# Performance work log

Hardware: AMD Instinct MI355X
Metric: run time of the kernel (lower is better)

## Reference

```python
import jax, jax.numpy as jnp
import numpy as np

M_DIM = 256.0  # scaling denominator from __init__ (sqrt(256) = 16)

def setup_inputs() -> dict:
    key = jax.random.key(0)
    kq, kk, kv = jax.random.split(key, 3)
    B, H, S, D = 2, 8, 4096, 64
    q = jax.random.normal(kq, (B, H, S, D), dtype=jnp.float32)
    k = jax.random.normal(kk, (B, H, S, D), dtype=jnp.float32)
    v = jax.random.normal(kv, (B, H, S, D), dtype=jnp.float32)
    return {"q": q, "k": k, "v": v}

def reference(q, k, v):
    # scores: [B, H, S, S] = q @ k^T / sqrt(m_dim)
    scores = jnp.einsum('bhqd,bhkd->bhqk', q, k) / jnp.sqrt(jnp.float32(M_DIM))
    attn = jax.nn.softmax(scores, axis=-1)
    # outputs: [B, H, S, D]
    return jnp.einsum('bhqk,bhkd->bhqd', attn, v)
```

## Files before the change

kernel.cpp:

```cpp
#include <hip/hip_runtime.h>
#include <hip/hip_bf16.h>
#include <stdint.h>

#define SEQ 4096
#define DH  64
#define KT  32
#define PS  40
#define NIT ((SEQ / 4) / KT)
#define QSCALE 0.090168440f

typedef __attribute__((ext_vector_type(8))) short short8;
typedef __attribute__((ext_vector_type(4))) float floatx4;

__device__ __forceinline__ ushort f2bf_rne(float f) {
    unsigned u = __float_as_uint(f);
    unsigned r = u + 0x7FFFu + ((u >> 16) & 1u);
    return (ushort)(r >> 16);
}

__global__ __launch_bounds__(256)
void prep_kv(const float* __restrict__ K, const float* __restrict__ V,
             ushort* __restrict__ Kf, ushort* __restrict__ Vf) {
    const int bh = blockIdx.y, kb0 = blockIdx.x * 128, t = threadIdx.x;
    const size_t inB = ((size_t)bh * SEQ + kb0) * DH;
    {
        const float* srcB = K + inB;
        ushort* dstB = Kf + (size_t)bh * SEQ * DH + (size_t)(kb0 >> 4) * 1024;
        #pragma unroll
        for (int p = 0; p < 4; ++p) {
            int c   = p * 256 + t;
            int g   = c >> 7, rem = c & 127;
            int tt  = rem >> 6, lam = rem & 63;
            int key = g * 16 + (lam & 15);
            int d0  = tt * 32 + (lam >> 4) * 8;
            const float* s = srcB + (size_t)key * DH + d0;
            float4 a = *(const float4*)s;
            float4 b = *(const float4*)(s + 4);
            short8 o;
            o[0] = (short)f2bf_rne(a.x); o[1] = (short)f2bf_rne(a.y);
            o[2] = (short)f2bf_rne(a.z); o[3] = (short)f2bf_rne(a.w);
            o[4] = (short)f2bf_rne(b.x); o[5] = (short)f2bf_rne(b.y);
            o[6] = (short)f2bf_rne(b.z); o[7] = (short)f2bf_rne(b.w);
            *(short8*)(dstB + g * 1024 + tt * 512 + lam * 8) = o;
        }
    }
    {
        const int d0 = (t & 15) * 4, sl = (t >> 4) * 8;
        const float* src = V + inB + (size_t)sl * DH + d0;
        ushort* dstB = Vf + (size_t)bh * SEQ * DH + (size_t)(kb0 >> 5) * 2048;
        ushort b[8][4];
        #pragma unroll
        for (int r = 0; r < 8; ++r) {
            float4 f = *(const float4*)(src + r * DH);
            b[r][0] = f2bf_rne(f.x); b[r][1] = f2bf_rne(f.y);
            b[r][2] = f2bf_rne(f.z); b[r][3] = f2bf_rne(f.w);
        }
        const int Tl = sl >> 5, kq = (sl & 31) >> 3;
        #pragma unroll
        for (int i = 0; i < 4; ++i) {
            int d = d0 + i;
            short8 w;
            #pragma unroll
            for (int r = 0; r < 8; ++r) w[r] = (short)b[r][i];
            *(short8*)(dstB + Tl * 2048 + (d >> 4) * 512 + kq * 128 + (d & 15) * 8) = w;
        }
    }
}

__global__ __launch_bounds__(256, 4)
void attn_fwd_v14(const float* __restrict__ Q, const ushort* __restrict__ Kf,
                  const ushort* __restrict__ Vf, float* __restrict__ O)
{
    __shared__ __align__(16) char smem[35328];

    const int g    = blockIdx.x;
    const int bh   = (g & 7) * 2 + ((g >> 3) & 1);
    const int qt0  = (g >> 4) * 64;

    const int tid   = threadIdx.x;
    const int wave  = tid >> 6;
    const int lane  = tid & 63;
    const int n16   = lane & 15;
    const int quad  = lane >> 4;

    const float* Qb  = Q + ((size_t)bh * SEQ) * DH;
    const char*  KfB = (const char*)(Kf + (size_t)bh * SEQ * DH);
    const char*  VfB = (const char*)(Vf + (size_t)bh * SEQ * DH);
    float*       Ob  = O + ((size_t)bh * SEQ) * DH;

    ushort* sPw = (ushort*)smem + wave * (64 * PS);
    ushort* sQ  = (ushort*)(smem + 20480);

    #pragma unroll
    for (int p = 0; p < 2; ++p) {
        int c   = p * 256 + tid;
        int qt  = c >> 7, rem = c & 127;
        int tt  = rem >> 6, lam = rem & 63;
        int row = qt0 + qt * 16 + (lam & 15);
        int d0  = tt * 32 + (lam >> 4) * 8;
        const float* s = Qb + (size_t)row * DH + d0;
        float4 a = *(const float4*)s;
        float4 b = *(const float4*)(s + 4);
        short8 o;
        o[0] = (short)f2bf_rne(a.x * QSCALE); o[1] = (short)f2bf_rne(a.y * QSCALE);
        o[2] = (short)f2bf_rne(a.z * QSCALE); o[3] = (short)f2bf_rne(a.w * QSCALE);
        o[4] = (short)f2bf_rne(b.x * QSCALE); o[5] = (short)f2bf_rne(b.y * QSCALE);
        o[6] = (short)f2bf_rne(b.z * QSCALE); o[7] = (short)f2bf_rne(b.w * QSCALE);
        *(short8*)(sQ + qt * 1024 + tt * 512 + lam * 8) = o;
    }

    floatx4 oacc[4][4];
    float   lpart[4];
    #pragma unroll
    for (int qt = 0; qt < 4; ++qt) {
        lpart[qt] = 0.f;
        #pragma unroll
        for (int nt = 0; nt < 4; ++nt) oacc[qt][nt] = (floatx4){0.f, 0.f, 0.f, 0.f};
    }

    const int wqoff = __builtin_amdgcn_readfirstlane(wave * 131072);
    const char* kpB = KfB + wqoff;
    const char* vpB = VfB + wqoff;
    const int lo = lane * 16;

    short8 kf[4];
    #pragma unroll
    for (int c = 0; c < 4; ++c) kf[c] = *(const short8*)(kpB + lo + c * 1024);

    __syncthreads();

    const ushort* sQl = sQ + lane * 8;

    int off = 0;
    #pragma unroll 1
    for (int it = 0; it < NIT; ++it) {
        asm volatile("" ::: "memory");

        const int offn = (it + 1 < NIT) ? off + 4096 : 0;

        #pragma unroll
        for (int qt = 0; qt < 4; ++qt) {
            short8 q0 = *(const short8*)(sQl + qt * 1024);
            short8 q1 = *(const short8*)(sQl + qt * 1024 + 512);
            floatx4 s0 = (floatx4){0.f, 0.f, 0.f, 0.f};
            floatx4 s1 = (floatx4){0.f, 0.f, 0.f, 0.f};
            __builtin_amdgcn_s_setprio(1);
            s0 = __builtin_amdgcn_mfma_f32_16x16x32_bf16(kf[0], q0, s0, 0, 0, 0);
            s0 = __builtin_amdgcn_mfma_f32_16x16x32_bf16(kf[1], q1, s0, 0, 0, 0);
            s1 = __builtin_amdgcn_mfma_f32_16x16x32_bf16(kf[2], q0, s1, 0, 0, 0);
            s1 = __builtin_amdgcn_mfma_f32_16x16x32_bf16(kf[3], q1, s1, 0, 0, 0);
            __builtin_amdgcn_s_setprio(0);
            {
                float e0 = __builtin_amdgcn_exp2f(s0[0]);
                float e1 = __builtin_amdgcn_exp2f(s0[1]);
                float e2 = __builtin_amdgcn_exp2f(s0[2]);
                float e3 = __builtin_amdgcn_exp2f(s0[3]);
                lpart[qt] += (e0 + e1) + (e2 + e3);
                uint2 w;
                w.x = __builtin_amdgcn_perm(__float_as_uint(e1), __float_as_uint(e0), 0x07060302);
                w.y = __builtin_amdgcn_perm(__float_as_uint(e3), __float_as_uint(e2), 0x07060302);
                *(uint2*)&sPw[(qt * 16 + n16) * PS + quad * 4] = w;
            }
            {
                float e0 = __builtin_amdgcn_exp2f(s1[0]);
                float e1 = __builtin_amdgcn_exp2f(s1[1]);
                float e2 = __builtin_amdgcn_exp2f(s1[2]);
                float e3 = __builtin_amdgcn_exp2f(s1[3]);
                lpart[qt] += (e0 + e1) + (e2 + e3);
                uint2 w;
                w.x = __builtin_amdgcn_perm(__float_as_uint(e1), __float_as_uint(e0), 0x07060302);
                w.y = __builtin_amdgcn_perm(__float_as_uint(e3), __float_as_uint(e2), 0x07060302);
                *(uint2*)&sPw[(qt * 16 + n16) * PS + 16 + quad * 4] = w;
            }
        }

        asm volatile("" ::: "memory");

        short8 vf[4];
        #pragma unroll
        for (int c = 0; c < 4; ++c) vf[c] = *(const short8*)(vpB + lo + off + c * 1024);

        #pragma unroll
        for (int c = 0; c < 4; ++c) kf[c] = *(const short8*)(kpB + lo + offn + c * 1024);

        #pragma unroll
        for (int qt = 0; qt < 4; ++qt) {
            short8 pfq = *(const short8*)&sPw[(qt * 16 + n16) * PS + quad * 8];
            __builtin_amdgcn_s_setprio(1);
            #pragma unroll
            for (int nt = 0; nt < 4; ++nt)
                oacc[qt][nt] = __builtin_amdgcn_mfma_f32_16x16x32_bf16(vf[nt], pfq, oacc[qt][nt], 0, 0, 0);
            __builtin_amdgcn_s_setprio(0);
        }

        off = offn;
    }

    float lq[4];
    #pragma unroll
    for (int qt = 0; qt < 4; ++qt) {
        float s = lpart[qt];
        s += __shfl_xor(s, 16, 64);
        s += __shfl_xor(s, 32, 64);
        lq[qt] = s;
    }

    __syncthreads();
    if (wave & 1) {
        char* rb = smem + (wave >> 1) * 17664;
        float* eO = (float*)rb;
        float* eL = (float*)(rb + 17408);
        #pragma unroll
        for (int qt = 0; qt < 4; ++qt) {
            const int row = qt * 16 + n16;
            #pragma unroll
            for (int nt = 0; nt < 4; ++nt)
                *(float4*)&eO[row * 68 + nt * 16 + quad * 4] = (float4){
                    oacc[qt][nt][0], oacc[qt][nt][1], oacc[qt][nt][2], oacc[qt][nt][3]};
            if (quad == 0) eL[row] = lq[qt];
        }
    }
    __syncthreads();
    if (!(wave & 1)) {
        const char* rb = smem + (wave >> 1) * 17664;
        const float* eO = (const float*)rb;
        const float* eL = (const float*)(rb + 17408);
        #pragma unroll
        for (int qt = 0; qt < 4; ++qt) {
            const int row = qt * 16 + n16;
            lq[qt] += eL[row];
            #pragma unroll
            for (int nt = 0; nt < 4; ++nt) {
                float4 part = *(const float4*)&eO[row * 68 + nt * 16 + quad * 4];
                oacc[qt][nt][0] += part.x; oacc[qt][nt][1] += part.y;
                oacc[qt][nt][2] += part.z; oacc[qt][nt][3] += part.w;
            }
        }
    }
    __syncthreads();
    if (wave == 2) {
        char* rb = smem;
        float* eO = (float*)rb;
        float* eL = (float*)(rb + 17408);
        #pragma unroll
        for (int qt = 0; qt < 4; ++qt) {
            const int row = qt * 16 + n16;
            #pragma unroll
            for (int nt = 0; nt < 4; ++nt)
                *(float4*)&eO[row * 68 + nt * 16 + quad * 4] = (float4){
                    oacc[qt][nt][0], oacc[qt][nt][1], oacc[qt][nt][2], oacc[qt][nt][3]};
            if (quad == 0) eL[row] = lq[qt];
        }
    }
    __syncthreads();
    if (wave == 0) {
        const float* eO = (const float*)smem;
        const float* eL = (const float*)(smem + 17408);
        #pragma unroll
        for (int qt = 0; qt < 4; ++qt) {
            const int row = qt * 16 + n16;
            const float inv = 1.0f / (lq[qt] + eL[row]);
            const int q = qt0 + row;
            #pragma unroll
            for (int nt = 0; nt < 4; ++nt) {
                float4 part = *(const float4*)&eO[row * 68 + nt * 16 + quad * 4];
                float4 o;
                o.x = (oacc[qt][nt][0] + part.x) * inv;
                o.y = (oacc[qt][nt][1] + part.y) * inv;
                o.z = (oacc[qt][nt][2] + part.z) * inv;
                o.w = (oacc[qt][nt][3] + part.w) * inv;
                *(float4*)&Ob[(size_t)q * DH + nt * 16 + quad * 4] = o;
            }
        }
    }
}

__global__ __launch_bounds__(256, 4)
void attn_fwd_v1(const float* __restrict__ Q, const float* __restrict__ K,
                 const float* __restrict__ V, float* __restrict__ O)
{
    __shared__ __align__(16) ushort sKf[64 * 72];
    __shared__ __align__(16) ushort sVf[64 * 72];
    __shared__ __align__(16) ushort sPf[4 * 16 * 72];
    const int bh = blockIdx.y, qt0 = blockIdx.x * 64, tid = threadIdx.x;
    const int wave = tid >> 6, lane = tid & 63, n16 = lane & 15, quad = lane >> 4;
    const size_t base = (size_t)bh * SEQ * DH;
    const float *Qb = Q + base, *Kb = K + base, *Vb = V + base;
    float* Ob = O + base;
    short8 qfrag[2];
    {
        const float* qrow = Qb + (size_t)(qt0 + wave * 16 + n16) * DH;
        #pragma unroll
        for (int t = 0; t < 2; ++t) {
            const float* p = qrow + t * 32 + quad * 8;
            short8 a;
            #pragma unroll
            for (int j = 0; j < 8; ++j) a[j] = (short)f2bf_rne(p[j] * 0.0625f);
            qfrag[t] = a;
        }
    }
    floatx4 oacc[4];
    #pragma unroll
    for (int nt = 0; nt < 4; ++nt) oacc[nt] = (floatx4){0.f,0.f,0.f,0.f};
    float m_i[4] = {-INFINITY,-INFINITY,-INFINITY,-INFINITY};
    float l_i[4] = {0.f,0.f,0.f,0.f};
    const int skr = tid >> 2, sc0 = (tid & 3) * 16;
    for (int kt0 = 0; kt0 < SEQ; kt0 += 64) {
        __syncthreads();
        const float* ksrc = Kb + (size_t)(kt0 + skr) * DH + sc0;
        const float* vsrc = Vb + (size_t)(kt0 + skr) * DH + sc0;
        ushort* kdst = &sKf[skr * 72 + sc0];
        #pragma unroll
        for (int i = 0; i < 16; i += 4) {
            float4 kf = *(const float4*)(ksrc + i);
            kdst[i+0]=f2bf_rne(kf.x); kdst[i+1]=f2bf_rne(kf.y);
            kdst[i+2]=f2bf_rne(kf.z); kdst[i+3]=f2bf_rne(kf.w);
            float4 vf = *(const float4*)(vsrc + i);
            sVf[(sc0+i+0)*72+skr]=f2bf_rne(vf.x); sVf[(sc0+i+1)*72+skr]=f2bf_rne(vf.y);
            sVf[(sc0+i+2)*72+skr]=f2bf_rne(vf.z); sVf[(sc0+i+3)*72+skr]=f2bf_rne(vf.w);
        }
        __syncthreads();
        floatx4 sacc[4];
        #pragma unroll
        for (int nt = 0; nt < 4; ++nt) {
            sacc[nt] = (floatx4){0.f,0.f,0.f,0.f};
            #pragma unroll
            for (int t = 0; t < 2; ++t) {
                short8 b = *(const short8*)&sKf[(nt*16+n16)*72 + t*32 + quad*8];
                sacc[nt] = __builtin_amdgcn_mfma_f32_16x16x32_bf16(qfrag[t], b, sacc[nt], 0,0,0);
            }
        }
        ushort* pw = &sPf[wave * 16 * 72];
        #pragma unroll
        for (int r = 0; r < 4; ++r) {
            float mx = fmaxf(fmaxf(sacc[0][r],sacc[1][r]),fmaxf(sacc[2][r],sacc[3][r]));
            #pragma unroll
            for (int off = 1; off < 16; off <<= 1) mx = fmaxf(mx, __shfl_xor(mx, off, 64));
            float mnew = fmaxf(m_i[r], mx);
            float alpha = __expf(m_i[r] - mnew);
            m_i[r] = mnew;
            float sum = 0.f;
            #pragma unroll
            for (int nt = 0; nt < 4; ++nt) {
                float p = __expf(sacc[nt][r] - mnew);
                sacc[nt][r] = p; sum += p;
            }
            #pragma unroll
            for (int off = 1; off < 16; off <<= 1) sum += __shfl_xor(sum, off, 64);
            l_i[r] = l_i[r] * alpha + sum;
            #pragma unroll
            for (int nt = 0; nt < 4; ++nt) oacc[nt][r] *= alpha;
            #pragma unroll
            for (int nt = 0; nt < 4; ++nt)
                pw[(quad*4+r)*72 + nt*16 + n16] = f2bf_rne(sacc[nt][r]);
        }
        #pragma unroll
        for (int t = 0; t < 2; ++t) {
            short8 pfr = *(const short8*)&pw[n16*72 + t*32 + quad*8];
            #pragma unroll
            for (int nt = 0; nt < 4; ++nt) {
                short8 vfr = *(const short8*)&sVf[(nt*16+n16)*72 + t*32 + quad*8];
                oacc[nt] = __builtin_amdgcn_mfma_f32_16x16x32_bf16(pfr, vfr, oacc[nt], 0,0,0);
            }
        }
    }
    #pragma unroll
    for (int r = 0; r < 4; ++r) {
        float inv = 1.0f / l_i[r];
        float* orow = Ob + (size_t)(qt0 + wave*16 + quad*4 + r) * DH;
        #pragma unroll
        for (int nt = 0; nt < 4; ++nt) orow[nt*16+n16] = oacc[nt][r] * inv;
    }
}

extern "C" void kernel_launch(void* const* d_in, const int* in_sizes, int n_in,
                              void* d_out, int out_size, void* d_ws, size_t ws_size,
                              hipStream_t stream) {
    const float* q = (const float*)d_in[0];
    const float* k = (const float*)d_in[1];
    const float* v = (const float*)d_in[2];
    float* o = (float*)d_out;
    const size_t elems = (size_t)16 * SEQ * DH;
    const size_t need  = elems * 2 * 2;
    if (ws_size >= need) {
        ushort* kf = (ushort*)d_ws;
        ushort* vf = kf + elems;
        prep_kv<<<dim3(SEQ / 128, 16), dim3(256), 0, stream>>>(k, v, kf, vf);
        attn_fwd_v14<<<dim3(1024), dim3(256), 0, stream>>>(q, kf, vf, o);
    } else {
        attn_fwd_v1<<<dim3(SEQ / 64, 16), dim3(256), 0, stream>>>(q, k, v, o);
    }
}
```

Baseline: 163.4 us.

## Keep softmax probabilities in registers by permuting V key order in prep

Removes the per-wave LDS round trip for the P tile. The exponentiated scores now go straight from the QK^T MFMA accumulator layout into the B operand of the PV MFMA, packed with v_cvt_pk_bf16_f32. To make this valid, prep_kv permutes the key ordering of the V fragments so the keys held by each lane match the accumulator row layout. This cuts LDS writes, reads and perm instructions in the inner loop, but relies on the key permutation being exactly consistent between the two kernels.

```diff
diff --git a/kernel.cpp b/kernel.cpp
--- a/kernel.cpp
+++ b/kernel.cpp
@@ -5,17 +5,23 @@
 #define SEQ 4096
 #define DH  64
 #define KT  32
-#define PS  40
 #define NIT ((SEQ / 4) / KT)
 #define QSCALE 0.090168440f
 
 typedef __attribute__((ext_vector_type(8))) short short8;
 typedef __attribute__((ext_vector_type(4))) float floatx4;
+typedef __attribute__((ext_vector_type(4))) unsigned uintx4;
 
 __device__ __forceinline__ ushort f2bf_rne(float f) {
     unsigned u = __float_as_uint(f);
     unsigned r = u + 0x7FFFu + ((u >> 16) & 1u);
     return (ushort)(r >> 16);
+}
+
+__device__ __forceinline__ unsigned cvt_pk_bf16(float lo, float hi) {
+    unsigned r;
+    asm("v_cvt_pk_bf16_f32 %0, %1, %2" : "=v"(r) : "v"(lo), "v"(hi));
+    return r;
 }
 
 __global__ __launch_bounds__(256)
@@ -46,16 +52,17 @@
     }
     {
         const int d0 = (t & 15) * 4, sl = (t >> 4) * 8;
-        const float* src = V + inB + (size_t)sl * DH + d0;
+        const int Tl = sl >> 5, kq = (sl & 31) >> 3;
+        const float* src = V + inB + (size_t)(Tl * 32 + kq * 4) * DH + d0;
         ushort* dstB = Vf + (size_t)bh * SEQ * DH + (size_t)(kb0 >> 5) * 2048;
         ushort b[8][4];
         #pragma unroll
         for (int r = 0; r < 8; ++r) {
-            float4 f = *(const float4*)(src + r * DH);
+            int row = ((r >> 2) << 4) + (r & 3);
+            float4 f = *(const float4*)(src + row * DH);
             b[r][0] = f2bf_rne(f.x); b[r][1] = f2bf_rne(f.y);
             b[r][2] = f2bf_rne(f.z); b[r][3] = f2bf_rne(f.w);
         }
-        const int Tl = sl >> 5, kq = (sl & 31) >> 3;
         #pragma unroll
         for (int i = 0; i < 4; ++i) {
             int d = d0 + i;
@@ -68,7 +75,7 @@
 }
 
 __global__ __launch_bounds__(256, 4)
-void attn_fwd_v14(const float* __restrict__ Q, const ushort* __restrict__ Kf,
+void attn_fwd_v15(const float* __restrict__ Q, const ushort* __restrict__ Kf,
                   const ushort* __restrict__ Vf, float* __restrict__ O)
 {
     __shared__ __align__(16) char smem[35328];
@@ -88,7 +95,6 @@
     const char*  VfB = (const char*)(Vf + (size_t)bh * SEQ * DH);
     float*       Ob  = O + ((size_t)bh * SEQ) * DH;
 
-    ushort* sPw = (ushort*)smem + wave * (64 * PS);
     ushort* sQ  = (ushort*)(smem + 20480);
 
     #pragma unroll
@@ -138,6 +144,7 @@
 
         const int offn = (it + 1 < NIT) ? off + 4096 : 0;
 
+        uintx4 pf4[4];
         #pragma unroll
         for (int qt = 0; qt < 4; ++qt) {
             short8 q0 = *(const short8*)(sQl + qt * 1024);
@@ -150,28 +157,19 @@
             s1 = __builtin_amdgcn_mfma_f32_16x16x32_bf16(kf[2], q0, s1, 0, 0, 0);
             s1 = __builtin_amdgcn_mfma_f32_16x16x32_bf16(kf[3], q1, s1, 0, 0, 0);
             __builtin_amdgcn_s_setprio(0);
-            {
-                float e0 = __builtin_amdgcn_exp2f(s0[0]);
-                float e1 = __builtin_amdgcn_exp2f(s0[1]);
-                float e2 = __builtin_amdgcn_exp2f(s0[2]);
-                float e3 = __builtin_amdgcn_exp2f(s0[3]);
-                lpart[qt] += (e0 + e1) + (e2 + e3);
-                uint2 w;
-                w.x = __builtin_amdgcn_perm(__float_as_uint(e1), __float_as_uint(e0), 0x07060302);
-                w.y = __builtin_amdgcn_perm(__float_as_uint(e3), __float_as_uint(e2), 0x07060302);
-                *(uint2*)&sPw[(qt * 16 + n16) * PS + quad * 4] = w;
-            }
-            {
-                float e0 = __builtin_amdgcn_exp2f(s1[0]);
-                float e1 = __builtin_amdgcn_exp2f(s1[1]);
-                float e2 = __builtin_amdgcn_exp2f(s1[2]);
-                float e3 = __builtin_amdgcn_exp2f(s1[3]);
-                lpart[qt] += (e0 + e1) + (e2 + e3);
-                uint2 w;
-                w.x = __builtin_amdgcn_perm(__float_as_uint(e1), __float_as_uint(e0), 0x07060302);
-                w.y = __builtin_amdgcn_perm(__float_as_uint(e3), __float_as_uint(e2), 0x07060302);
-                *(uint2*)&sPw[(qt * 16 + n16) * PS + 16 + quad * 4] = w;
-            }
+            float e00 = __builtin_amdgcn_exp2f(s0[0]);
+            float e01 = __builtin_amdgcn_exp2f(s0[1]);
+            float e02 = __builtin_amdgcn_exp2f(s0[2]);
+            float e03 = __builtin_amdgcn_exp2f(s0[3]);
+            float e10 = __builtin_amdgcn_exp2f(s1[0]);
+            float e11 = __builtin_amdgcn_exp2f(s1[1]);
+            float e12 = __builtin_amdgcn_exp2f(s1[2]);
+            float e13 = __builtin_amdgcn_exp2f(s1[3]);
+            lpart[qt] += ((e00 + e01) + (e02 + e03)) + ((e10 + e11) + (e12 + e13));
+            pf4[qt][0] = cvt_pk_bf16(e00, e01);
+            pf4[qt][1] = cvt_pk_bf16(e02, e03);
+            pf4[qt][2] = cvt_pk_bf16(e10, e11);
+            pf4[qt][3] = cvt_pk_bf16(e12, e13);
         }
 
         asm volatile("" ::: "memory");
@@ -185,11 +183,12 @@
 
         #pragma unroll
         for (int qt = 0; qt < 4; ++qt) {
-            short8 pfq = *(const short8*)&sPw[(qt * 16 + n16) * PS + quad * 8];
+            union { uintx4 u; short8 s; } pc;
+            pc.u = pf4[qt];
             __builtin_amdgcn_s_setprio(1);
             #pragma unroll
             for (int nt = 0; nt < 4; ++nt)
-                oacc[qt][nt] = __builtin_amdgcn_mfma_f32_16x16x32_bf16(vf[nt], pfq, oacc[qt][nt], 0, 0, 0);
+                oacc[qt][nt] = __builtin_amdgcn_mfma_f32_16x16x32_bf16(vf[nt], pc.s, oacc[qt][nt], 0, 0, 0);
             __builtin_amdgcn_s_setprio(0);
         }
 
@@ -386,7 +385,7 @@
         ushort* kf = (ushort*)d_ws;
         ushort* vf = kf + elems;
         prep_kv<<<dim3(SEQ / 128, 16), dim3(256), 0, stream>>>(k, v, kf, vf);
-        attn_fwd_v14<<<dim3(1024), dim3(256), 0, stream>>>(q, kf, vf, o);
+        attn_fwd_v15<<<dim3(1024), dim3(256), 0, stream>>>(q, kf, vf, o);
     } else {
         attn_fwd_v1<<<dim3(SEQ / 64, 16), dim3(256), 0, stream>>>(q, k, v, o);
     }
```

After: 160.9 us. No clear change (-1.5%).
